# Kernel optimization log

Measured on AMD Instinct MI355X. Metric: run time of the kernel, lower is better.

The kernel has to match this reference:

```python
import jax, jax.numpy as jnp
import numpy as np

B, C, D, E = 2048, 64, 1024, 128
P_INT = 0.0  # p_int=0 -> intervention mask is all zeros (deterministic)


def setup_inputs() -> dict:
    key = jax.random.key(0)
    ks = jax.random.split(key, 16)
    s = lambda k, shape, fan: jax.random.normal(k, shape, jnp.float32) * (1.0 / np.sqrt(fan))
    return {
        "x": jax.random.normal(ks[0], (B, D), jnp.float32),
        "c_int": jax.random.uniform(ks[1], (B, C), jnp.float32),
        # stacked per-concept scorer MLP: Linear(D,D) -> ReLU -> Linear(D,1) -> Sigmoid
        "W1": s(ks[2], (C, D, D), D), "b1": jnp.zeros((C, D), jnp.float32),
        "w2": s(ks[3], (C, D), D), "b2": jnp.zeros((C,), jnp.float32),
        # stacked per-concept embed layer: Linear(D+1, D+1) -> ReLU
        "Wl": s(ks[4], (C, D + 1, D + 1), D + 1), "bl": jnp.zeros((C, D + 1), jnp.float32),
        # shared heads
        "Wmu": s(ks[5], (D + 1, E), D + 1), "bmu": jnp.zeros((E,), jnp.float32),
        "Wlv": s(ks[6], (D + 1, E), D + 1), "blv": jnp.zeros((E,), jnp.float32),
        "proto_pos": jax.random.normal(ks[7], (C, E), jnp.float32),
        "proto_neg": jax.random.normal(ks[8], (C, E), jnp.float32),
    }


def reference(x, c_int, W1, b1, w2, b2, Wl, bl, Wmu, bmu, Wlv, blv, proto_pos, proto_neg):
    # Concept scorers (all concepts batched as one grouped GEMM).
    h = jax.nn.relu(jnp.einsum("bd,cdk->bck", x, W1) + b1)          # [B,C,D]
    c_pred = jax.nn.sigmoid(jnp.einsum("bck,ck->bc", h, w2) + b2)    # [B,C]
    # Per-concept embedding layer on [x ; c_pred].
    xc = jnp.concatenate(
        [jnp.broadcast_to(x[:, None, :], (x.shape[0], C, D)), c_pred[..., None]], axis=-1
    )                                                                # [B,C,D+1]
    emb = jax.nn.relu(jnp.einsum("bck,ckj->bcj", xc, Wl) + bl)       # [B,C,D+1]
    mu = jnp.einsum("bcj,je->bce", emb, Wmu) + bmu                   # [B,C,E]
    logvar = jnp.einsum("bcj,je->bce", emb, Wlv) + blv               # [B,C,E]
    c_emb = mu  # eval mode: no reparameterization noise
    # Intervention blend (mask ~ Bernoulli(p_int); p_int=0 -> zeros, deterministic)
    mask = jnp.zeros_like(c_pred)                                    # [B,C]
    cp = mask * c_int + (1.0 - mask) * c_pred                        # [B,C]
    proto = cp[..., None] * proto_pos + (1.0 - cp[..., None]) * proto_neg  # [B,C,E]
    c_emb = mask[..., None] * proto + (1.0 - mask[..., None]) * c_emb
    return (c_pred, c_emb, mu, logvar)
```

## Files before the change

kernel.cpp:

```cpp
#include <hip/hip_runtime.h>
#include <hip/hip_bf16.h>
#include <cstdint>
#include <cstddef>

#define NP 1152

#define OFF_CE 131072ull
#define OFF_MU (131072ull + 16777216ull)
#define OFF_LV (131072ull + 33554432ull)

using bf16x8 = __attribute__((ext_vector_type(8))) __bf16;
using s16x8  = __attribute__((ext_vector_type(8))) short;
using f32x4  = __attribute__((ext_vector_type(4))) float;

__device__ __forceinline__ unsigned short f2bf(float x) {
  unsigned u = __builtin_bit_cast(unsigned, x);
  return (unsigned short)((u + 0x7FFFu + ((u >> 16) & 1u)) >> 16);
}
__device__ __forceinline__ float bf2f(unsigned short h) {
  unsigned u = ((unsigned)h) << 16;
  return __builtin_bit_cast(float, u);
}
__device__ __forceinline__ void async16(const void* g, void* l) {
  __builtin_amdgcn_global_load_lds(
      (const __attribute__((address_space(1))) void*)g,
      (__attribute__((address_space(3))) void*)l, 16, 0, 0);
}


__global__ __launch_bounds__(256) void convert_x_k(const float* __restrict__ x,
                                                   unsigned short* __restrict__ xb) {
  int idx = blockIdx.x * 256 + threadIdx.x;
  const float4* xv = (const float4*)x;
  float4 a = xv[idx * 2], b = xv[idx * 2 + 1];
  unsigned w0 = f2bf(a.x) | ((unsigned)f2bf(a.y) << 16);
  unsigned w1 = f2bf(a.z) | ((unsigned)f2bf(a.w) << 16);
  unsigned w2 = f2bf(b.x) | ((unsigned)f2bf(b.y) << 16);
  unsigned w3 = f2bf(b.z) | ((unsigned)f2bf(b.w) << 16);
  ((uint4*)xb)[idx] = make_uint4(w0, w1, w2, w3);
}

__global__ void transpose_w1_k(const float* __restrict__ src0, unsigned short* __restrict__ dst0) {
  __shared__ float t[32][33];
  const int c = blockIdx.z;
  const int k0 = blockIdx.x << 5, n0 = blockIdx.y << 5;
  const int tx = threadIdx.x, ty = threadIdx.y;
  const float* src = src0 + ((size_t)c << 20);
#pragma unroll
  for (int r = 0; r < 4; ++r)
    t[ty + (r << 3)][tx] = src[((size_t)(k0 + ty + (r << 3)) << 10) + n0 + tx];
  __syncthreads();
  unsigned short* dst = dst0 + ((size_t)c << 20);
#pragma unroll
  for (int r = 0; r < 4; ++r)
    dst[((size_t)(n0 + ty + (r << 3)) << 10) + k0 + tx] = f2bf(t[tx][ty + (r << 3)]);
}

__global__ void transpose_wl_k(const float* __restrict__ Wl, unsigned short* __restrict__ WlT) {
  __shared__ float t[32][33];
  const int c = blockIdx.z;
  const int k0 = blockIdx.x << 5, n0 = blockIdx.y << 5;
  const int tx = threadIdx.x, ty = threadIdx.y;
  const float* src = Wl + (size_t)c * 1025 * 1025;
#pragma unroll
  for (int r = 0; r < 4; ++r) {
    int k = k0 + ty + (r << 3);
    int n = n0 + tx;
    t[ty + (r << 3)][tx] = (n < 1025) ? src[(size_t)k * 1025 + n] : 0.f;
  }
  __syncthreads();
  unsigned short* dst = WlT + (size_t)c * NP * 1024;
#pragma unroll
  for (int r = 0; r < 4; ++r)
    dst[(size_t)(n0 + ty + (r << 3)) * 1024 + k0 + tx] = f2bf(t[tx][ty + (r << 3)]);
}

__global__ __launch_bounds__(256) void wlast_blp_k(const float* __restrict__ Wl,
                                                   const float* __restrict__ bl,
                                                   float* __restrict__ wlastf,
                                                   float* __restrict__ blpf) {
  int idx = blockIdx.x * 256 + threadIdx.x;
  int c = idx / NP, n = idx - c * NP;
  wlastf[idx] = (n < 1025) ? Wl[((size_t)c * 1025 + 1024) * 1025 + n] : 0.f;
  blpf[idx]   = (n < 1025) ? bl[(size_t)c * 1025 + n] : 0.f;
}

__global__ __launch_bounds__(256) void convert_whead_k(const float* __restrict__ Wmu,
                                                       const float* __restrict__ Wlv,
                                                       unsigned short* __restrict__ WheadT) {
  int idx = blockIdx.x * 256 + threadIdx.x;
  int rr = idx / NP, k = idx - rr * NP;
  float v = 0.f;
  if (k < 1025) v = (rr < 128) ? Wmu[(size_t)k * 128 + rr] : Wlv[(size_t)k * 128 + (rr - 128)];
  WheadT[idx] = f2bf(v);
}


__global__ __launch_bounds__(256) void scorer_k(const unsigned short* __restrict__ h,
                                                const float* __restrict__ w2,
                                                const float* __restrict__ b2,
                                                float* __restrict__ pred_out,
                                                float* __restrict__ cpf) {
  int wv = (blockIdx.x << 2) + (threadIdx.x >> 6);
  int lane = threadIdx.x & 63;
  int c = wv >> 11, b = wv & 2047;
  const unsigned short* hr = h + ((size_t)wv << 10);
  const float* wr = w2 + (c << 10);
  float s = 0.f;
#pragma unroll
  for (int ch = 0; ch < 2; ++ch) {
    int base = ch * 512 + lane * 8;
    s16x8 hv = *(const s16x8*)(hr + base);
    float4 w0 = *(const float4*)(wr + base);
    float4 w1 = *(const float4*)(wr + base + 4);
    s += bf2f((unsigned short)hv[0]) * w0.x + bf2f((unsigned short)hv[1]) * w0.y +
         bf2f((unsigned short)hv[2]) * w0.z + bf2f((unsigned short)hv[3]) * w0.w +
         bf2f((unsigned short)hv[4]) * w1.x + bf2f((unsigned short)hv[5]) * w1.y +
         bf2f((unsigned short)hv[6]) * w1.z + bf2f((unsigned short)hv[7]) * w1.w;
  }
#pragma unroll
  for (int off = 32; off; off >>= 1) s += __shfl_xor(s, off);
  if (lane == 0) {
    float p = 1.f / (1.f + expf(-(s + b2[c])));
    pred_out[((size_t)b << 6) + c] = p;
    cpf[((size_t)b << 6) + c] = p;
  }
}


#define BAR() __builtin_amdgcn_s_barrier()
#define LGKM0() do { asm volatile("s_waitcnt lgkmcnt(0)" ::: "memory"); \
                     __builtin_amdgcn_sched_barrier(0); } while (0)
#define VM4() asm volatile("s_waitcnt vmcnt(4)" ::: "memory")

#define STAGEA(h, tt, bidx) do { _Pragma("unroll") for (int q_ = 0; q_ < 2; ++q_) \
  async16(Asrc[q_] + ((size_t)(h) * 128) * K + (size_t)(tt) * 64, \
          &sA[bidx][(h) * 8192 + chnk[q_]]); } while (0)
#define STAGEB(h, tt, bidx) do { _Pragma("unroll") for (int q_ = 0; q_ < 2; ++q_) \
  async16(Bsrc[q_] + ((size_t)(h) * 128) * K + (size_t)(tt) * 64, \
          &sB[bidx][(h) * 8192 + chnk[q_]]); } while (0)

#define LOADA(mh, bidx) do { _Pragma("unroll") for (int i_ = 0; i_ < 4; ++i_) { \
  const int ro_ = ((mh) * 128 + wm64 + i_ * 16 + l15) << 6; \
  a[i_][0] = *(const bf16x8*)&sA[bidx][ro_ + ccx0]; \
  a[i_][1] = *(const bf16x8*)&sA[bidx][ro_ + ccx1]; } } while (0)

#define LOADB(nh, bb, bidx) do { _Pragma("unroll") for (int j_ = 0; j_ < 2; ++j_) { \
  const int ro_ = ((nh) * 128 + wn32 + j_ * 16 + l15) << 6; \
  bb[j_][0] = *(const bf16x8*)&sB[bidx][ro_ + ccx0]; \
  bb[j_][1] = *(const bf16x8*)&sB[bidx][ro_ + ccx1]; } } while (0)

#define MMAQ(mh, nh, bb) do { _Pragma("unroll") for (int i_ = 0; i_ < 4; ++i_) \
  _Pragma("unroll") for (int j_ = 0; j_ < 2; ++j_) { \
    acc[(mh)*4+i_][(nh)*2+j_] = __builtin_amdgcn_mfma_f32_16x16x32_bf16( \
        a[i_][0], bb[j_][0], acc[(mh)*4+i_][(nh)*2+j_], 0, 0, 0); \
    acc[(mh)*4+i_][(nh)*2+j_] = __builtin_amdgcn_mfma_f32_16x16x32_bf16( \
        a[i_][1], bb[j_][1], acc[(mh)*4+i_][(nh)*2+j_], 0, 0, 0); \
  } } while (0)

template <int MODE>
__global__ __launch_bounds__(512, 2) void gemm8p_k(
    const unsigned short* __restrict__ A, const unsigned short* __restrict__ BT, const int K,
    const float* __restrict__ e0, const float* __restrict__ e1, const float* __restrict__ e2,
    unsigned short* __restrict__ obf, float* __restrict__ ofl) {
  __shared__ unsigned short sA[2][16384];
  __shared__ unsigned short sB[2][16384];

  constexpr int GX = (MODE == 2) ? 1 : (MODE == 1) ? 5 : 4;
  constexpr int GY = (MODE == 2) ? 512 : 8;
  constexpr int NWG = GX * GY * ((MODE == 2) ? 1 : 64);

  const int tid = threadIdx.x;
  const int lane = tid & 63;
  const int wid = tid >> 6;
  const int wm = wid >> 2, wn = wid & 3;
  const int l15 = lane & 15, l4 = lane >> 4;
  const int wm64 = wm << 6, wn32 = wn << 5;

  const int rbid = blockIdx.x + GX * (blockIdx.y + GY * blockIdx.z);
  const int bid = (rbid & 7) * (NWG >> 3) + (rbid >> 3);
  const int bx = bid % GX;
  const int by = (bid / GX) % GY;
  const int c = bid / (GX * GY);

  int n0 = bx << 8;
  if constexpr (MODE == 1) { if (n0 > NP - 256) n0 = NP - 256; }
  const int m0 = by << 8;

  const unsigned short* Ab = A;
  const unsigned short* Bb;
  if constexpr (MODE == 0)      Bb = BT + ((size_t)c << 20);
  else if constexpr (MODE == 1) Bb = BT + (size_t)c * (NP * 1024);
  else                          Bb = BT;

  int rloc[2], csrc[2], chnk[2];
  const unsigned short* Asrc[2];
  const unsigned short* Bsrc[2];
#pragma unroll
  for (int q = 0; q < 2; ++q) {
    const int s = ((wid << 1) + q) * 64 + lane;
    rloc[q] = s >> 3;
    csrc[q] = ((s & 7) ^ ((s >> 3) & 7)) << 3;
    chnk[q] = ((wid << 1) + q) << 9;
    Asrc[q] = Ab + (size_t)(m0 + rloc[q]) * K + csrc[q];
    Bsrc[q] = Bb + (size_t)(n0 + rloc[q]) * K + csrc[q];
  }

  const int xorv = l15 & 7;
  const int ccx0 = (l4 ^ xorv) << 3;
  const int ccx1 = ((4 + l4) ^ xorv) << 3;

  f32x4 acc[8][4];
#pragma unroll
  for (int i = 0; i < 8; ++i)
#pragma unroll
    for (int j = 0; j < 4; ++j) acc[i][j] = (f32x4)(0.f);

  bf16x8 a[4][2], b0[2][2], b1[2][2];

  const int nt = K >> 6;

  STAGEA(0, 0, 0); STAGEB(0, 0, 0); STAGEB(1, 0, 0); STAGEA(1, 0, 0);
  asm volatile("s_waitcnt vmcnt(0)" ::: "memory");
  BAR();

  for (int t = 0; t < nt; ++t) {
    const int cb = t & 1, nb = cb ^ 1;
    const bool pf = (t + 1 < nt);
    LOADA(0, cb);
    LOADB(0, b0, cb);
    if (pf) STAGEA(0, t + 1, nb);
    BAR();
    LGKM0();
    __builtin_amdgcn_s_setprio(1);
    MMAQ(0, 0, b0);
    __builtin_amdgcn_s_setprio(0);
    VM4();
    BAR();
    LOADB(1, b1, cb);
    if (pf) STAGEB(0, t + 1, nb);
    BAR();
    LGKM0();
    __builtin_amdgcn_s_setprio(1);
    MMAQ(0, 1, b1);
    __builtin_amdgcn_s_setprio(0);
    VM4();
    BAR();
    LOADA(1, cb);
    if (pf) STAGEB(1, t + 1, nb);
    BAR();
    LGKM0();
    __builtin_amdgcn_s_setprio(1);
    MMAQ(1, 1, b1);
    __builtin_amdgcn_s_setprio(0);
    BAR();
    if (pf) STAGEA(1, t + 1, nb);
    BAR();
    __builtin_amdgcn_s_setprio(1);
    MMAQ(1, 0, b0);
    __builtin_amdgcn_s_setprio(0);
    VM4();
    BAR();
  }

  int coln[2][2];
#pragma unroll
  for (int nh = 0; nh < 2; ++nh)
#pragma unroll
    for (int j = 0; j < 2; ++j) coln[nh][j] = n0 + nh * 128 + wn32 + j * 16 + l15;

  if constexpr (MODE == 0) {
    float bias[2][2];
#pragma unroll
    for (int nh = 0; nh < 2; ++nh)
#pragma unroll
      for (int j = 0; j < 2; ++j) bias[nh][j] = e0[(c << 10) + coln[nh][j]];
#pragma unroll
    for (int mh = 0; mh < 2; ++mh)
#pragma unroll
      for (int i = 0; i < 4; ++i)
#pragma unroll
        for (int rr = 0; rr < 4; ++rr) {
          const int row = m0 + mh * 128 + wm64 + i * 16 + (l4 << 2) + rr;
          unsigned short* orow = obf + ((size_t)((c << 11) + row) << 10);
#pragma unroll
          for (int nh = 0; nh < 2; ++nh)
#pragma unroll
            for (int j = 0; j < 2; ++j) {
              float v = acc[mh * 4 + i][nh * 2 + j][rr] + bias[nh][j];
              orow[coln[nh][j]] = f2bf(fmaxf(v, 0.f));
            }
        }
  } else if constexpr (MODE == 1) {
    float wl4[2][2], bb4[2][2];
#pragma unroll
    for (int nh = 0; nh < 2; ++nh)
#pragma unroll
      for (int j = 0; j < 2; ++j) {
        wl4[nh][j] = e0[c * NP + coln[nh][j]];
        bb4[nh][j] = e1[c * NP + coln[nh][j]];
      }
#pragma unroll
    for (int mh = 0; mh < 2; ++mh)
#pragma unroll
      for (int i = 0; i < 4; ++i)
#pragma unroll
        for (int rr = 0; rr < 4; ++rr) {
          const int row = m0 + mh * 128 + wm64 + i * 16 + (l4 << 2) + rr;
          const float cp = e2[((size_t)row << 6) + c];
          unsigned short* orow = obf + (size_t)((c << 11) + row) * NP;
#pragma unroll
          for (int nh = 0; nh < 2; ++nh)
#pragma unroll
            for (int j = 0; j < 2; ++j) {
              float v = acc[mh * 4 + i][nh * 2 + j][rr] + cp * wl4[nh][j] + bb4[nh][j];
              orow[coln[nh][j]] = f2bf(fmaxf(v, 0.f));
            }
        }
  } else {
    float bias[2][2];
#pragma unroll
    for (int nh = 0; nh < 2; ++nh)
#pragma unroll
      for (int j = 0; j < 2; ++j)
        bias[nh][j] = (nh == 0) ? e0[coln[0][j]] : e1[coln[1][j] - 128];
#pragma unroll
    for (int mh = 0; mh < 2; ++mh)
#pragma unroll
      for (int i = 0; i < 4; ++i)
#pragma unroll
        for (int rr = 0; rr < 4; ++rr) {
          const int rid = m0 + mh * 128 + wm64 + i * 16 + (l4 << 2) + rr;
          const int cc = rid >> 11, b = rid & 2047;
          const size_t ib = (((size_t)b << 6) + cc) << 7;
#pragma unroll
          for (int j = 0; j < 2; ++j) {
            float v = acc[mh * 4 + i][j][rr] + bias[0][j];
            ofl[OFF_MU + ib + coln[0][j]] = v;
            ofl[OFF_CE + ib + coln[0][j]] = v;
          }
#pragma unroll
          for (int j = 0; j < 2; ++j) {
            float v = acc[mh * 4 + i][2 + j][rr] + bias[1][j];
            ofl[OFF_LV + ib + (coln[1][j] - 128)] = v;
          }
        }
  }
}


extern "C" void kernel_launch(void* const* d_in, const int* in_sizes, int n_in,
                              void* d_out, int out_size, void* d_ws, size_t ws_size,
                              hipStream_t stream) {
  const float* x   = (const float*)d_in[0];
  const float* W1  = (const float*)d_in[2];
  const float* b1  = (const float*)d_in[3];
  const float* w2  = (const float*)d_in[4];
  const float* b2  = (const float*)d_in[5];
  const float* Wl  = (const float*)d_in[6];
  const float* bl  = (const float*)d_in[7];
  const float* Wmu = (const float*)d_in[8];
  const float* bmu = (const float*)d_in[9];
  const float* Wlv = (const float*)d_in[10];
  const float* blv = (const float*)d_in[11];
  float* out = (float*)d_out;

  char* ws = (char*)d_ws;
  unsigned short* xb     = (unsigned short*)(ws);
  unsigned short* WT     = (unsigned short*)(ws + 4194304ull);
  float* wlastf          = (float*)(ws + 155189248ull);
  float* blpf            = (float*)(ws + 155484160ull);
  unsigned short* WheadT = (unsigned short*)(ws + 155779072ull);
  float* cpf             = (float*)(ws + 156368896ull);
  unsigned short* hemb   = (unsigned short*)(ws + 156893184ull);

  convert_x_k<<<1024, 256, 0, stream>>>(x, xb);
  transpose_w1_k<<<dim3(32, 32, 64), dim3(32, 8), 0, stream>>>(W1, WT);
  gemm8p_k<0><<<dim3(4, 8, 64), 512, 0, stream>>>(xb, WT, 1024, b1, nullptr, nullptr, hemb, nullptr);
  scorer_k<<<32768, 256, 0, stream>>>(hemb, w2, b2, out, cpf);
  transpose_wl_k<<<dim3(32, 36, 64), dim3(32, 8), 0, stream>>>(Wl, WT);
  wlast_blp_k<<<288, 256, 0, stream>>>(Wl, bl, wlastf, blpf);
  convert_whead_k<<<1152, 256, 0, stream>>>(Wmu, Wlv, WheadT);
  gemm8p_k<1><<<dim3(5, 8, 64), 512, 0, stream>>>(xb, WT, 1024, wlastf, blpf, cpf, hemb, nullptr);
  gemm8p_k<2><<<dim3(1, 512, 1), 512, 0, stream>>>(hemb, WheadT, 1152, bmu, blv, nullptr, nullptr, out);
}
```

Baseline: 1.038 ms.

## Fuse scorer dot into GEMM epilogue and peel padded column 1024

The first grouped GEMM's epilogue now applies ReLU and reduces against w2 in registers and LDS, writing per-N-tile partial sums instead of a full bf16 h tensor. A small sigmoid kernel then combines the partials. The extra embedding column 1024 is computed separately by a column GEMV plus sigmoid step and folded into the head GEMM epilogue as a rank-1 update. This lets the embed GEMM and head GEMM run on an exact 1024 width instead of padded 1152 tiles. The GEMM main loop also peels its last iteration to drop the prefetch predicate. Together these remove a large h write/read round trip and about 12% of padded MMA and transpose work, at the cost of more small launches and a low-parallelism GEMV over only 64 blocks.

```diff
diff --git a/kernel.cpp b/kernel.cpp
--- a/kernel.cpp
+++ b/kernel.cpp
@@ -2,8 +2,6 @@
 #include <hip/hip_bf16.h>
 #include <cstdint>
 #include <cstddef>
-
-#define NP 1152
 
 #define OFF_CE 131072ull
 #define OFF_MU (131072ull + 16777216ull)
@@ -63,68 +61,100 @@
   const int tx = threadIdx.x, ty = threadIdx.y;
   const float* src = Wl + (size_t)c * 1025 * 1025;
 #pragma unroll
-  for (int r = 0; r < 4; ++r) {
-    int k = k0 + ty + (r << 3);
-    int n = n0 + tx;
-    t[ty + (r << 3)][tx] = (n < 1025) ? src[(size_t)k * 1025 + n] : 0.f;
-  }
+  for (int r = 0; r < 4; ++r)
+    t[ty + (r << 3)][tx] = src[(size_t)(k0 + ty + (r << 3)) * 1025 + n0 + tx];
   __syncthreads();
-  unsigned short* dst = WlT + (size_t)c * NP * 1024;
+  unsigned short* dst = WlT + ((size_t)c << 20);
 #pragma unroll
   for (int r = 0; r < 4; ++r)
-    dst[(size_t)(n0 + ty + (r << 3)) * 1024 + k0 + tx] = f2bf(t[tx][ty + (r << 3)]);
-}
-
-__global__ __launch_bounds__(256) void wlast_blp_k(const float* __restrict__ Wl,
-                                                   const float* __restrict__ bl,
-                                                   float* __restrict__ wlastf,
-                                                   float* __restrict__ blpf) {
+    dst[((size_t)(n0 + ty + (r << 3)) << 10) + k0 + tx] = f2bf(t[tx][ty + (r << 3)]);
+}
+
+__global__ __launch_bounds__(256) void prep_wl_k(const float* __restrict__ Wl,
+                                                 const float* __restrict__ bl,
+                                                 float* __restrict__ wlastf,
+                                                 float* __restrict__ blpf,
+                                                 float* __restrict__ Wlcolf,
+                                                 float* __restrict__ w2l,
+                                                 float* __restrict__ bl1024) {
   int idx = blockIdx.x * 256 + threadIdx.x;
-  int c = idx / NP, n = idx - c * NP;
-  wlastf[idx] = (n < 1025) ? Wl[((size_t)c * 1025 + 1024) * 1025 + n] : 0.f;
-  blpf[idx]   = (n < 1025) ? bl[(size_t)c * 1025 + n] : 0.f;
+  int c = idx >> 10, j = idx & 1023;
+  const float* src = Wl + (size_t)c * 1025 * 1025;
+  wlastf[idx] = src[(size_t)1024 * 1025 + j];
+  blpf[idx]   = bl[(size_t)c * 1025 + j];
+  Wlcolf[idx] = src[(size_t)j * 1025 + 1024];
+  if (j == 0) {
+    w2l[c]    = src[(size_t)1024 * 1025 + 1024];
+    bl1024[c] = bl[(size_t)c * 1025 + 1024];
+  }
 }
 
 __global__ __launch_bounds__(256) void convert_whead_k(const float* __restrict__ Wmu,
                                                        const float* __restrict__ Wlv,
-                                                       unsigned short* __restrict__ WheadT) {
+                                                       unsigned short* __restrict__ WheadT,
+                                                       float* __restrict__ whead1024f) {
   int idx = blockIdx.x * 256 + threadIdx.x;
-  int rr = idx / NP, k = idx - rr * NP;
-  float v = 0.f;
-  if (k < 1025) v = (rr < 128) ? Wmu[(size_t)k * 128 + rr] : Wlv[(size_t)k * 128 + (rr - 128)];
+  int rr = idx >> 10, k = idx & 1023;
+  float v = (rr < 128) ? Wmu[(size_t)k * 128 + rr] : Wlv[(size_t)k * 128 + (rr - 128)];
   WheadT[idx] = f2bf(v);
-}
-
-
-__global__ __launch_bounds__(256) void scorer_k(const unsigned short* __restrict__ h,
-                                                const float* __restrict__ w2,
-                                                const float* __restrict__ b2,
-                                                float* __restrict__ pred_out,
-                                                float* __restrict__ cpf) {
-  int wv = (blockIdx.x << 2) + (threadIdx.x >> 6);
-  int lane = threadIdx.x & 63;
-  int c = wv >> 11, b = wv & 2047;
-  const unsigned short* hr = h + ((size_t)wv << 10);
-  const float* wr = w2 + (c << 10);
-  float s = 0.f;
-#pragma unroll
-  for (int ch = 0; ch < 2; ++ch) {
-    int base = ch * 512 + lane * 8;
-    s16x8 hv = *(const s16x8*)(hr + base);
-    float4 w0 = *(const float4*)(wr + base);
-    float4 w1 = *(const float4*)(wr + base + 4);
-    s += bf2f((unsigned short)hv[0]) * w0.x + bf2f((unsigned short)hv[1]) * w0.y +
-         bf2f((unsigned short)hv[2]) * w0.z + bf2f((unsigned short)hv[3]) * w0.w +
-         bf2f((unsigned short)hv[4]) * w1.x + bf2f((unsigned short)hv[5]) * w1.y +
-         bf2f((unsigned short)hv[6]) * w1.z + bf2f((unsigned short)hv[7]) * w1.w;
-  }
-#pragma unroll
-  for (int off = 32; off; off >>= 1) s += __shfl_xor(s, off);
-  if (lane == 0) {
-    float p = 1.f / (1.f + expf(-(s + b2[c])));
-    pred_out[((size_t)b << 6) + c] = p;
-    cpf[((size_t)b << 6) + c] = p;
-  }
+  if (blockIdx.x == 0 && threadIdx.x < 256) {
+    int r2 = threadIdx.x;
+    whead1024f[r2] = (r2 < 128) ? Wmu[(size_t)1024 * 128 + r2] : Wlv[(size_t)1024 * 128 + (r2 - 128)];
+  }
+}
+
+__global__ __launch_bounds__(256) void colgemv_k(const unsigned short* __restrict__ xb,
+                                                 const float* __restrict__ Wlcolf,
+                                                 float* __restrict__ presum) {
+  __shared__ unsigned short xt[32 * 1024];
+  const int r0 = blockIdx.x << 5;
+  const int tid = threadIdx.x;
+#pragma unroll
+  for (int i = 0; i < 16; ++i)
+    ((uint4*)xt)[tid * 16 + i] = ((const uint4*)(xb + (size_t)r0 * 1024))[tid * 16 + i];
+  __syncthreads();
+  const int wv = tid >> 6, lane = tid & 63;
+  for (int c = 0; c < 64; ++c) {
+    float4 w[4];
+#pragma unroll
+    for (int q = 0; q < 4; ++q)
+      w[q] = *(const float4*)(Wlcolf + (c << 10) + lane * 16 + q * 4);
+#pragma unroll
+    for (int rr = 0; rr < 8; ++rr) {
+      const int r = (wv << 3) + rr;
+      const unsigned short* xr = xt + (r << 10) + lane * 16;
+      s16x8 h0 = *(const s16x8*)xr;
+      s16x8 h1 = *(const s16x8*)(xr + 8);
+      float s = 0.f;
+#pragma unroll
+      for (int i = 0; i < 8; ++i) {
+        s += bf2f((unsigned short)h0[i]) * ((const float*)&w[i >> 2])[i & 3];
+        s += bf2f((unsigned short)h1[i]) * ((const float*)&w[2 + (i >> 2)])[i & 3];
+      }
+#pragma unroll
+      for (int off = 32; off; off >>= 1) s += __shfl_xor(s, off);
+      if (lane == 0) presum[(c << 11) + r0 + r] = s;
+    }
+  }
+}
+
+__global__ __launch_bounds__(256) void sigmoid_k(const float* __restrict__ spart,
+                                                 const float* __restrict__ b2,
+                                                 const float* __restrict__ presum,
+                                                 const float* __restrict__ w2l,
+                                                 const float* __restrict__ bl1024,
+                                                 float* __restrict__ pred_out,
+                                                 float* __restrict__ cpf,
+                                                 float* __restrict__ e1024f) {
+  int idx = blockIdx.x * 256 + threadIdx.x;
+  int b = idx >> 6, c = idx & 63;
+  float s = b2[c];
+#pragma unroll
+  for (int q = 0; q < 4; ++q) s += spart[(((size_t)(q << 6) + c) << 11) + b];
+  float p = 1.f / (1.f + expf(-s));
+  pred_out[idx] = p;
+  cpf[idx] = p;
+  e1024f[(c << 11) + b] = fmaxf(presum[(c << 11) + b] + p * w2l[c] + bl1024[c], 0.f);
 }
 
 
@@ -132,6 +162,7 @@
 #define LGKM0() do { asm volatile("s_waitcnt lgkmcnt(0)" ::: "memory"); \
                      __builtin_amdgcn_sched_barrier(0); } while (0)
 #define VM4() asm volatile("s_waitcnt vmcnt(4)" ::: "memory")
+#define VM0() asm volatile("s_waitcnt vmcnt(0)" ::: "memory")
 
 #define STAGEA(h, tt, bidx) do { _Pragma("unroll") for (int q_ = 0; q_ < 2; ++q_) \
   async16(Asrc[q_] + ((size_t)(h) * 128) * K + (size_t)(tt) * 64, \
@@ -161,12 +192,13 @@
 template <int MODE>
 __global__ __launch_bounds__(512, 2) void gemm8p_k(
     const unsigned short* __restrict__ A, const unsigned short* __restrict__ BT, const int K,
-    const float* __restrict__ e0, const float* __restrict__ e1, const float* __restrict__ e2,
+    const float* __restrict__ e0, const float* __restrict__ e1,
+    const float* __restrict__ e2, const float* __restrict__ e3,
     unsigned short* __restrict__ obf, float* __restrict__ ofl) {
   __shared__ unsigned short sA[2][16384];
   __shared__ unsigned short sB[2][16384];
 
-  constexpr int GX = (MODE == 2) ? 1 : (MODE == 1) ? 5 : 4;
+  constexpr int GX = (MODE == 2) ? 1 : 4;
   constexpr int GY = (MODE == 2) ? 512 : 8;
   constexpr int NWG = GX * GY * ((MODE == 2) ? 1 : 64);
 
@@ -183,15 +215,13 @@
   const int by = (bid / GX) % GY;
   const int c = bid / (GX * GY);
 
-  int n0 = bx << 8;
-  if constexpr (MODE == 1) { if (n0 > NP - 256) n0 = NP - 256; }
+  const int n0 = bx << 8;
   const int m0 = by << 8;
 
   const unsigned short* Ab = A;
   const unsigned short* Bb;
-  if constexpr (MODE == 0)      Bb = BT + ((size_t)c << 20);
-  else if constexpr (MODE == 1) Bb = BT + (size_t)c * (NP * 1024);
-  else                          Bb = BT;
+  if constexpr (MODE == 2) Bb = BT;
+  else                     Bb = BT + ((size_t)c << 20);
 
   int rloc[2], csrc[2], chnk[2];
   const unsigned short* Asrc[2];
@@ -221,15 +251,14 @@
   const int nt = K >> 6;
 
   STAGEA(0, 0, 0); STAGEB(0, 0, 0); STAGEB(1, 0, 0); STAGEA(1, 0, 0);
-  asm volatile("s_waitcnt vmcnt(0)" ::: "memory");
+  VM0();
   BAR();
 
-  for (int t = 0; t < nt; ++t) {
+  for (int t = 0; t < nt - 1; ++t) {
     const int cb = t & 1, nb = cb ^ 1;
-    const bool pf = (t + 1 < nt);
     LOADA(0, cb);
     LOADB(0, b0, cb);
-    if (pf) STAGEA(0, t + 1, nb);
+    STAGEA(0, t + 1, nb);
     BAR();
     LGKM0();
     __builtin_amdgcn_s_setprio(1);
@@ -238,7 +267,7 @@
     VM4();
     BAR();
     LOADB(1, b1, cb);
-    if (pf) STAGEB(0, t + 1, nb);
+    STAGEB(0, t + 1, nb);
     BAR();
     LGKM0();
     __builtin_amdgcn_s_setprio(1);
@@ -247,14 +276,14 @@
     VM4();
     BAR();
     LOADA(1, cb);
-    if (pf) STAGEB(1, t + 1, nb);
+    STAGEB(1, t + 1, nb);
     BAR();
     LGKM0();
     __builtin_amdgcn_s_setprio(1);
     MMAQ(1, 1, b1);
     __builtin_amdgcn_s_setprio(0);
     BAR();
-    if (pf) STAGEA(1, t + 1, nb);
+    STAGEA(1, t + 1, nb);
     BAR();
     __builtin_amdgcn_s_setprio(1);
     MMAQ(1, 0, b0);
@@ -263,6 +292,29 @@
     BAR();
   }
 
+  {
+    const int cb = (nt - 1) & 1;
+    VM0();
+    BAR();
+    LOADA(0, cb);
+    LOADB(0, b0, cb);
+    LGKM0();
+    __builtin_amdgcn_s_setprio(1);
+    MMAQ(0, 0, b0);
+    __builtin_amdgcn_s_setprio(0);
+    LOADB(1, b1, cb);
+    LGKM0();
+    __builtin_amdgcn_s_setprio(1);
+    MMAQ(0, 1, b1);
+    __builtin_amdgcn_s_setprio(0);
+    LOADA(1, cb);
+    LGKM0();
+    __builtin_amdgcn_s_setprio(1);
+    MMAQ(1, 1, b1);
+    MMAQ(1, 0, b0);
+    __builtin_amdgcn_s_setprio(0);
+  }
+
   int coln[2][2];
 #pragma unroll
   for (int nh = 0; nh < 2; ++nh)
@@ -270,35 +322,50 @@
     for (int j = 0; j < 2; ++j) coln[nh][j] = n0 + nh * 128 + wn32 + j * 16 + l15;
 
   if constexpr (MODE == 0) {
-    float bias[2][2];
+    float bias[2][2], w2v[2][2];
 #pragma unroll
     for (int nh = 0; nh < 2; ++nh)
 #pragma unroll
-      for (int j = 0; j < 2; ++j) bias[nh][j] = e0[(c << 10) + coln[nh][j]];
+      for (int j = 0; j < 2; ++j) {
+        bias[nh][j] = e0[(c << 10) + coln[nh][j]];
+        w2v[nh][j]  = e1[(c << 10) + coln[nh][j]];
+      }
+    float* partL = (float*)&sA[0][0];
 #pragma unroll
     for (int mh = 0; mh < 2; ++mh)
 #pragma unroll
       for (int i = 0; i < 4; ++i)
 #pragma unroll
         for (int rr = 0; rr < 4; ++rr) {
-          const int row = m0 + mh * 128 + wm64 + i * 16 + (l4 << 2) + rr;
-          unsigned short* orow = obf + ((size_t)((c << 11) + row) << 10);
+          float s = 0.f;
 #pragma unroll
           for (int nh = 0; nh < 2; ++nh)
 #pragma unroll
             for (int j = 0; j < 2; ++j) {
-              float v = acc[mh * 4 + i][nh * 2 + j][rr] + bias[nh][j];
-              orow[coln[nh][j]] = f2bf(fmaxf(v, 0.f));
+              float v = fmaxf(acc[mh * 4 + i][nh * 2 + j][rr] + bias[nh][j], 0.f);
+              s += v * w2v[nh][j];
             }
+          s += __shfl_xor(s, 1); s += __shfl_xor(s, 2);
+          s += __shfl_xor(s, 4); s += __shfl_xor(s, 8);
+          if (l15 == 0) partL[wid * 128 + mh * 64 + i * 16 + (l4 << 2) + rr] = s;
         }
+    __syncthreads();
+    if (tid < 256) {
+      const int r = tid;
+      const int mh_ = r >> 7, wmr = (r >> 6) & 1, low = r & 63;
+      float s2 = 0.f;
+#pragma unroll
+      for (int wn2 = 0; wn2 < 4; ++wn2) s2 += partL[(wmr * 4 + wn2) * 128 + mh_ * 64 + low];
+      ofl[(((size_t)(bx << 6) + c) << 11) + m0 + r] = s2;
+    }
   } else if constexpr (MODE == 1) {
     float wl4[2][2], bb4[2][2];
 #pragma unroll
     for (int nh = 0; nh < 2; ++nh)
 #pragma unroll
       for (int j = 0; j < 2; ++j) {
-        wl4[nh][j] = e0[c * NP + coln[nh][j]];
-        bb4[nh][j] = e1[c * NP + coln[nh][j]];
+        wl4[nh][j] = e0[(c << 10) + coln[nh][j]];
+        bb4[nh][j] = e1[(c << 10) + coln[nh][j]];
       }
 #pragma unroll
     for (int mh = 0; mh < 2; ++mh)
@@ -308,7 +375,7 @@
         for (int rr = 0; rr < 4; ++rr) {
           const int row = m0 + mh * 128 + wm64 + i * 16 + (l4 << 2) + rr;
           const float cp = e2[((size_t)row << 6) + c];
-          unsigned short* orow = obf + (size_t)((c << 11) + row) * NP;
+          unsigned short* orow = obf + (((size_t)(c << 11) + row) << 10);
 #pragma unroll
           for (int nh = 0; nh < 2; ++nh)
 #pragma unroll
@@ -318,12 +385,14 @@
             }
         }
   } else {
-    float bias[2][2];
+    float bias[2][2], wh[2][2];
 #pragma unroll
     for (int nh = 0; nh < 2; ++nh)
 #pragma unroll
-      for (int j = 0; j < 2; ++j)
+      for (int j = 0; j < 2; ++j) {
         bias[nh][j] = (nh == 0) ? e0[coln[0][j]] : e1[coln[1][j] - 128];
+        wh[nh][j]   = e3[coln[nh][j]];
+      }
 #pragma unroll
     for (int mh = 0; mh < 2; ++mh)
 #pragma unroll
@@ -332,16 +401,17 @@
         for (int rr = 0; rr < 4; ++rr) {
           const int rid = m0 + mh * 128 + wm64 + i * 16 + (l4 << 2) + rr;
           const int cc = rid >> 11, b = rid & 2047;
+          const float ev = e2[rid];
           const size_t ib = (((size_t)b << 6) + cc) << 7;
 #pragma unroll
           for (int j = 0; j < 2; ++j) {
-            float v = acc[mh * 4 + i][j][rr] + bias[0][j];
+            float v = acc[mh * 4 + i][j][rr] + bias[0][j] + ev * wh[0][j];
             ofl[OFF_MU + ib + coln[0][j]] = v;
             ofl[OFF_CE + ib + coln[0][j]] = v;
           }
 #pragma unroll
           for (int j = 0; j < 2; ++j) {
-            float v = acc[mh * 4 + i][2 + j][rr] + bias[1][j];
+            float v = acc[mh * 4 + i][2 + j][rr] + bias[1][j] + ev * wh[1][j];
             ofl[OFF_LV + ib + (coln[1][j] - 128)] = v;
           }
         }
@@ -368,19 +438,30 @@
   char* ws = (char*)d_ws;
   unsigned short* xb     = (unsigned short*)(ws);
   unsigned short* WT     = (unsigned short*)(ws + 4194304ull);
-  float* wlastf          = (float*)(ws + 155189248ull);
-  float* blpf            = (float*)(ws + 155484160ull);
-  unsigned short* WheadT = (unsigned short*)(ws + 155779072ull);
-  float* cpf             = (float*)(ws + 156368896ull);
-  unsigned short* hemb   = (unsigned short*)(ws + 156893184ull);
+  float* wlastf          = (float*)(ws + 138412032ull);
+  float* blpf            = (float*)(ws + 138674176ull);
+  float* Wlcolf          = (float*)(ws + 138936320ull);
+  float* w2l             = (float*)(ws + 139198464ull);
+  float* bl1024          = (float*)(ws + 139198720ull);
+  unsigned short* WheadT = (unsigned short*)(ws + 139198976ull);
+  float* whead1024f      = (float*)(ws + 139723264ull);
+  float* presum          = (float*)(ws + 139724288ull);
+  float* spart           = (float*)(ws + 140248576ull);
+  float* cpf             = (float*)(ws + 142345728ull);
+  float* e1024f          = (float*)(ws + 142870016ull);
+  unsigned short* emb    = (unsigned short*)(ws + 143394304ull);
 
   convert_x_k<<<1024, 256, 0, stream>>>(x, xb);
   transpose_w1_k<<<dim3(32, 32, 64), dim3(32, 8), 0, stream>>>(W1, WT);
-  gemm8p_k<0><<<dim3(4, 8, 64), 512, 0, stream>>>(xb, WT, 1024, b1, nullptr, nullptr, hemb, nullptr);
-  scorer_k<<<32768, 256, 0, stream>>>(hemb, w2, b2, out, cpf);
-  transpose_wl_k<<<dim3(32, 36, 64), dim3(32, 8), 0, stream>>>(Wl, WT);
-  wlast_blp_k<<<288, 256, 0, stream>>>(Wl, bl, wlastf, blpf);
-  convert_whead_k<<<1152, 256, 0, stream>>>(Wmu, Wlv, WheadT);
-  gemm8p_k<1><<<dim3(5, 8, 64), 512, 0, stream>>>(xb, WT, 1024, wlastf, blpf, cpf, hemb, nullptr);
-  gemm8p_k<2><<<dim3(1, 512, 1), 512, 0, stream>>>(hemb, WheadT, 1152, bmu, blv, nullptr, nullptr, out);
-}
+  prep_wl_k<<<256, 256, 0, stream>>>(Wl, bl, wlastf, blpf, Wlcolf, w2l, bl1024);
+  convert_whead_k<<<1024, 256, 0, stream>>>(Wmu, Wlv, WheadT, whead1024f);
+  colgemv_k<<<64, 256, 0, stream>>>(xb, Wlcolf, presum);
+  gemm8p_k<0><<<dim3(4, 8, 64), 512, 0, stream>>>(xb, WT, 1024, b1, w2, nullptr, nullptr,
+                                                  nullptr, spart);
+  sigmoid_k<<<512, 256, 0, stream>>>(spart, b2, presum, w2l, bl1024, out, cpf, e1024f);
+  transpose_wl_k<<<dim3(32, 32, 64), dim3(32, 8), 0, stream>>>(Wl, WT);
+  gemm8p_k<1><<<dim3(4, 8, 64), 512, 0, stream>>>(xb, WT, 1024, wlastf, blpf, cpf, nullptr,
+                                                  emb, nullptr);
+  gemm8p_k<2><<<dim3(1, 512, 1), 512, 0, stream>>>(emb, WheadT, 1024, bmu, blv, e1024f,
+                                                   whead1024f, nullptr, out);
+}
```

Result: slower. 1.117 ms (+7.6%).
